# Performance work log

Measured on AMD Instinct MI355X. Metric: run time of the kernel, lower is better.

Reference implementation:

```python
import jax, jax.numpy as jnp
import numpy as np

# MLABlock dims (from __init__ defaults / chosen init_kwargs)
B, S, D = 2, 2048, 2048
H = 16
NOPE, ROPE, VD = 128, 64, 128
KVR = 512
NE, TOPK = 12, 4
EI, SEI = 1024, 2048
THETA = 10000.0
MSCALE = 1.0
EPS = 1e-6


def setup_inputs() -> dict:
    key = jax.random.key(0)
    ks = jax.random.split(key, 14)
    w = lambda k, shp: jax.random.normal(k, shp, jnp.float32) * 0.02
    return {
        "x": jax.random.normal(ks[0], (B, S, D), jnp.float32),
        "start_pos": 0,
        "norm_w": jnp.ones((D,), jnp.float32),
        "wq": w(ks[1], (H * (NOPE + ROPE), D)),
        "wkv_a": w(ks[2], (KVR + ROPE, D)),
        "kv_norm_w": jnp.ones((KVR,), jnp.float32),
        "wkv_b": w(ks[3], (H * (NOPE + VD), KVR)),
        "wo": w(ks[4], (D, H * VD)),
        "gate_w": w(ks[5], (NE, D)),
        "gate_bias": w(ks[6], (NE,)),
        "w1": w(ks[7], (NE, EI, D)),
        "w2": w(ks[8], (NE, D, EI)),
        "w3": w(ks[9], (NE, EI, D)),
        "sw1": w(ks[10], (SEI, D)),
        "sw2": w(ks[11], (D, SEI)),
        "sw3": w(ks[12], (SEI, D)),
    }


def _rms(v, w):
    return v * jax.lax.rsqrt(jnp.mean(v * v, -1, keepdims=True) + EPS) * w


def reference(x, start_pos, norm_w, wq, wkv_a, kv_norm_w, wkv_b, wo,
              gate_w, gate_bias, w1, w2, w3, sw1, sw2, sw3):
    b, s, d = x.shape
    # ---- MLA attention sub-layer ----
    h = _rms(x, norm_w)
    q = (h @ wq.T).reshape(b, s, H, NOPE + ROPE)
    q_nope, q_pe = q[..., :NOPE], q[..., NOPE:]
    kv = h @ wkv_a.T                      # [b,s,KVR+ROPE]
    kv_lat, k_pe = kv[..., :KVR], kv[..., KVR:]
    # rotary embedding (interleaved pairs), positions start_pos..start_pos+s
    pos = jnp.arange(s, dtype=jnp.float32) + start_pos
    inv = 1.0 / (THETA ** (jnp.arange(0, ROPE, 2, dtype=jnp.float32) / ROPE))
    ang = pos[:, None] * inv              # [s, ROPE/2]
    cos = jnp.cos(ang)[None, :, None, :]
    sin = jnp.sin(ang)[None, :, None, :]
    def rot(t):                           # t: [b,s,h,ROPE]
        t1, t2 = t[..., 0::2], t[..., 1::2]
        return jnp.stack([t1 * cos - t2 * sin, t1 * sin + t2 * cos], -1).reshape(t.shape)
    q_pe = rot(q_pe)
    k_pe = rot(k_pe[:, :, None, :])       # [b,s,1,ROPE] shared across heads
    kv_lat = _rms(kv_lat, kv_norm_w)
    kvb = (kv_lat @ wkv_b.T).reshape(b, s, H, NOPE + VD)
    k_nope, v = kvb[..., :NOPE], kvb[..., NOPE:]
    k = jnp.concatenate([k_nope, jnp.broadcast_to(k_pe, (b, s, H, ROPE))], -1)
    qf = jnp.concatenate([q_nope, q_pe], -1)
    scale = MSCALE * (NOPE + ROPE) ** -0.5
    mask = jnp.triu(jnp.full((s, s), -1e9, x.dtype), 1)  # causal
    scores = jnp.einsum('bqhd,bkhd->bhqk', qf, k) * scale + mask
    attn = jax.nn.softmax(scores, -1)
    o = jnp.einsum('bhqk,bkhd->bqhd', attn, v).reshape(b, s, H * VD) @ wo.T
    first = o + x
    # ---- MoE sub-layer (shared self.norm reused) ----
    h2 = _rms(first, norm_w)
    g_scores = jax.nn.sigmoid(h2 @ gate_w.T)             # [b,s,NE]
    _, idx = jax.lax.top_k(g_scores + gate_bias, TOPK)   # adaptive-bias selection
    gw = jnp.take_along_axis(g_scores, idx, -1)          # weights from raw scores
    gw = gw / jnp.sum(gw, -1, keepdims=True)
    out = (jax.nn.silu(h2 @ sw1.T) * (h2 @ sw3.T)) @ sw2.T  # shared expert
    for e in range(NE):                                  # fixed small expert set
        we = jnp.sum(jnp.where(idx == e, gw, 0.0), -1)   # [b,s]
        ye = (jax.nn.silu(h2 @ w1[e].T) * (h2 @ w3[e].T)) @ w2[e].T
        out = out + we[..., None] * ye
    return out + first
```

## Files before the change

### kernel.cpp

```cpp
#include <hip/hip_runtime.h>
#include <cstdint>
#include <cstddef>
#include <cmath>

#define DI __device__ __forceinline__
typedef float f32x4 __attribute__((ext_vector_type(4)));
typedef __bf16 bf16x8 __attribute__((ext_vector_type(8)));
typedef unsigned short u16;
typedef unsigned int u32;

static constexpr int TKN = 4096, SEQ = 2048, DIM = 2048, NH = 16;

DI u16 f2bf(float f) {
  union { float f; u32 u; } v; v.f = f;
  u32 r = v.u + 0x7fffu + ((v.u >> 16) & 1u);
  return (u16)(r >> 16);
}
DI float bf2f(u16 h) {
  union { u32 u; float f; } v; v.u = ((u32)h) << 16;
  return v.f;
}
DI f32x4 mfma16(bf16x8 a, bf16x8 b, f32x4 c) {
  return __builtin_amdgcn_mfma_f32_16x16x32_bf16(a, b, c, 0, 0, 0);
}
DI void gld16(const u16* g, u16* l) {
  __builtin_amdgcn_global_load_lds((const __attribute__((address_space(1))) u32*)g,
                                   (__attribute__((address_space(3))) u32*)l, 16, 0, 0);
}

enum { EF_F32 = 0, EF_BF16 = 1, EF_RES = 2, EF_KV = 3, EF_SILU = 4, EF_ATOM = 5, EF_QROPE = 6 };
enum { AM_DIR = 0, AM_LIST = 1, AM_OFF = 2 };

template<int EPI, int AMODE, int NSEG>
__global__ __launch_bounds__(256)
void gemm_f(const u16* __restrict__ A, const u16* __restrict__ B, void* __restrict__ C,
            int M, int N, int K, size_t apl, size_t bpl,
            const int* __restrict__ list, const int* __restrict__ basep,
            const int* __restrict__ counts,
            const void* __restrict__ aux, const float* __restrict__ gws,
            u16* __restrict__ kd0, u16* __restrict__ kd1, u16* __restrict__ vT,
            const float* __restrict__ cosT)
{
  constexpr int BM = 128, BK = 64;
  __shared__ __align__(16) u16 As[BM * BK];
  __shared__ __align__(16) u16 Bs[BM * BK];
  int rowbase = 0;
  if (AMODE != AM_DIR) {
    int z = blockIdx.z;
    M = counts[z];
    rowbase = basep[z];
    B += (size_t)z * (size_t)N * K;
  }
  int m0 = blockIdx.x * BM, n0 = blockIdx.y * BM;
  if (m0 >= M) return;
  int tid = threadIdx.x, lane = tid & 63, wid = tid >> 6;
  int wm = (wid >> 1) * 64, wn = (wid & 1) * 64;
  int lr = lane & 15, lk = (lane >> 4) * 8;

  const u16* asrc[4];
  const u16* bsrc[4];
  int l8 = lane >> 3, c8 = ((lane & 7) ^ l8) * 8;
  #pragma unroll
  for (int i = 0; i < 4; i++) {
    int chunk = wid * 4 + i;
    int ra = m0 + chunk * 8 + l8;
    size_t rowidx;
    if (AMODE == AM_LIST)      rowidx = (size_t)list[rowbase + (ra < M ? ra : 0)];
    else if (AMODE == AM_OFF)  rowidx = (size_t)(rowbase + (ra < M ? ra : 0));
    else                       rowidx = (size_t)ra;
    asrc[i] = A + rowidx * (size_t)K + c8;
    int rb = n0 + chunk * 8 + l8;
    if (rb >= N) rb = N - 1;
    bsrc[i] = B + (size_t)rb * K + c8;
  }

  f32x4 acc[4][4] = {};
  int sw = lr & 7;
  #pragma unroll 1
  for (int s = 0; s < NSEG; s++) {
    int sa = (s == 4) ? 2 : (s & 1);
    int sb = (s == 5) ? 2 : ((s >> 1) & 1);
    size_t ao = (size_t)sa * apl, bo = (size_t)sb * bpl;
    for (int kt = 0; kt < K; kt += BK) {
      #pragma unroll
      for (int i = 0; i < 4; i++) {
        gld16(asrc[i] + ao + kt, &As[(wid * 4 + i) * 512]);
        gld16(bsrc[i] + bo + kt, &Bs[(wid * 4 + i) * 512]);
      }
      __syncthreads();
      #pragma unroll
      for (int ko = 0; ko < BK; ko += 32) {
        bf16x8 af[4], bv[4];
        int sl = ((((ko + lk) >> 3) ^ sw) << 3);
        #pragma unroll
        for (int i = 0; i < 4; i++)
          af[i] = *(const bf16x8*)(&As[(wm + i * 16 + lr) * 64 + sl]);
        #pragma unroll
        for (int j = 0; j < 4; j++)
          bv[j] = *(const bf16x8*)(&Bs[(wn + j * 16 + lr) * 64 + sl]);
        #pragma unroll
        for (int i = 0; i < 4; i++)
          #pragma unroll
          for (int j = 0; j < 4; j++)
            acc[i][j] = mfma16(af[i], bv[j], acc[i][j]);
      }
      __syncthreads();
    }
  }

  int og = (lane >> 4) * 4;
  #pragma unroll
  for (int i = 0; i < 4; i++)
    #pragma unroll
    for (int p = 0; p < 4; p++) {
      int r = m0 + wm + i * 16 + og + p;
      if (EPI != EF_QROPE && EPI != EF_KV) { if (r >= M) continue; }
      size_t outr = (AMODE == AM_DIR) ? (size_t)r : (size_t)(rowbase + r);
      #pragma unroll
      for (int j = 0; j < 4; j++) {
        int c = n0 + wn + j * 16 + lr;
        float v = acc[i][j][p];
        if (EPI == EF_F32) {
          if (c < N) ((float*)C)[outr * N + c] = v;
        } else if (EPI == EF_BF16) {
          ((u16*)C)[outr * N + c] = f2bf(v);
        } else if (EPI == EF_RES) {
          ((float*)C)[outr * N + c] = v + ((const float*)aux)[outr * N + c];
        } else if (EPI == EF_SILU) {
          float t = bf2f(((const u16*)aux)[outr * N + c]);
          float sg = t / (1.f + __expf(-t));
          ((u16*)C)[outr * N + c] = f2bf(sg * v);
        } else if (EPI == EF_ATOM) {
          int tok = list[outr];
          float w = gws[outr];
          atomicAdd((float*)C + (size_t)tok * N + c, w * v);
        } else if (EPI == EF_QROPE) {
          int wi = c % 192;
          float vo = v;
          if (wi >= 128) {
            float part = __shfl_xor(v, 1);
            int jj = (wi - 128) >> 1;
            int srow = r & (SEQ - 1);
            float cs = cosT[srow * 32 + jj];
            float sn = ((const float*)aux)[srow * 32 + jj];
            vo = (c & 1) ? (part * sn + v * cs) : (v * cs - part * sn);
          }
          u16 b0 = f2bf(vo);
          u16 b1 = f2bf(vo - bf2f(b0));
          kd0[outr * (size_t)N + c] = b0;
          kd1[outr * (size_t)N + c] = b1;
        } else if (EPI == EF_KV) {
          int hd = c >> 8, cc = c & 255;
          u16 b0 = f2bf(v);
          float r1 = v - bf2f(b0);
          u16 b1 = f2bf(r1);
          if (cc < 128) {
            size_t base = ((size_t)r * NH + hd) * 128 + cc;
            kd0[base] = b0; kd1[base] = b1;
          } else {
            u16 b2 = f2bf(r1 - bf2f(b1));
            int bb = r >> 11, ss = r & (SEQ - 1);
            constexpr size_t VPL = (size_t)32 * 128 * 2048;
            size_t vb = ((size_t)((bb * 16 + hd) * 128 + (cc - 128))) * 2048 + ss;
            vT[vb] = b0; vT[VPL + vb] = b1; vT[2 * VPL + vb] = b2;
          }
        }
      }
    }
}

__global__ __launch_bounds__(256)
void attn3(const u16* __restrict__ q0p, const u16* __restrict__ q1p,
           const u16* __restrict__ k0p, const u16* __restrict__ k1p,
           const u16* __restrict__ kp0, const u16* __restrict__ kp1,
           const u16* __restrict__ vT, u16* __restrict__ o0, float scale)
{
  constexpr int KLD = 200, VLD = 40, PLD = 36;
  constexpr size_t VPL = (size_t)32 * 128 * 2048;
  constexpr size_t OPL = (size_t)TKN * DIM;
  __shared__ __align__(16) u16 Ks[2][32 * KLD];
  __shared__ __align__(16) u16 Vt[3][128 * VLD];
  __shared__ __align__(16) float Ps[4][16 * PLD];

  int bh = blockIdx.y;
  int b = bh >> 4, h = bh & 15;
  int tid = threadIdx.x, lane = tid & 63, wid = tid >> 6;
  int lr = lane & 15, lg = lane >> 4, lk = lg * 8;
  size_t tbase = (size_t)b * SEQ;
  const u16* vbase = vT + (size_t)bh * 128 * 2048;

  for (int half = 0; half < 2; half++) {
    int qt = half ? (31 - (int)blockIdx.x) : (int)blockIdx.x;
    int q0r = qt * 64;
    bf16x8 qf[2][6];
    {
      size_t qoff = (tbase + q0r + wid * 16 + lr) * (size_t)3072 + h * 192;
      #pragma unroll
      for (int kc = 0; kc < 6; kc++) {
        qf[0][kc] = *(const bf16x8*)(q0p + qoff + kc * 32 + lk);
        qf[1][kc] = *(const bf16x8*)(q1p + qoff + kc * 32 + lk);
      }
    }
    f32x4 oacc[8] = {};
    float mrow[4], lrow[4];
    #pragma unroll
    for (int p = 0; p < 4; p++) { mrow[p] = -1e30f; lrow[p] = 0.f; }

    int nkt = 2 * qt + 2;
    for (int kt = 0; kt < nkt; kt++) {
      __syncthreads();
      int kr0 = kt * 32;
      #pragma unroll
      for (int p = 0; p < 2; p++) {
        const u16* knp = p ? k1p : k0p;
        const u16* kpp = p ? kp1 : kp0;
        #pragma unroll
        for (int i = 0; i < 2; i++) {
          int vv = tid + i * 256, r = vv >> 4, cc8 = (vv & 15) * 8;
          int4 d = *(const int4*)(knp + ((tbase + kr0 + r) * (size_t)NH + h) * 128 + cc8);
          *(int4*)(&Ks[p][r * KLD + cc8]) = d;
        }
        {
          int r = tid >> 3, cc8 = (tid & 7) * 8;
          int4 d = *(const int4*)(kpp + (tbase + kr0 + r) * (size_t)64 + cc8);
          *(int4*)(&Ks[p][r * KLD + 128 + cc8]) = d;
        }
      }
      #pragma unroll
      for (int p = 0; p < 3; p++) {
        #pragma unroll
        for (int i = 0; i < 2; i++) {
          int vv = tid + i * 256, d = vv >> 2, cc8 = (vv & 3) * 8;
          int4 dd = *(const int4*)(vbase + p * VPL + (size_t)d * 2048 + kr0 + cc8);
          *(int4*)(&Vt[p][d * VLD + cc8]) = dd;
        }
      }
      __syncthreads();

      f32x4 sacc[2] = {};
      #pragma unroll
      for (int j = 0; j < 2; j++)
        #pragma unroll
        for (int kc = 0; kc < 6; kc++) {
          bf16x8 kf0 = *(const bf16x8*)(&Ks[0][(j * 16 + lr) * KLD + kc * 32 + lk]);
          bf16x8 kf1 = *(const bf16x8*)(&Ks[1][(j * 16 + lr) * KLD + kc * 32 + lk]);
          f32x4 t = sacc[j];
          t = mfma16(qf[0][kc], kf0, t);
          t = mfma16(qf[1][kc], kf0, t);
          t = mfma16(qf[0][kc], kf1, t);
          sacc[j] = t;
        }

      bool tail = (kt >= 2 * qt);
      float fsc[4];
      #pragma unroll
      for (int p = 0; p < 4; p++) {
        float s0 = sacc[0][p] * scale, s1 = sacc[1][p] * scale;
        if (tail) {
          int qrow = q0r + wid * 16 + lg * 4 + p;
          if (kr0 + lr > qrow) s0 = -1e30f;
          if (kr0 + 16 + lr > qrow) s1 = -1e30f;
        }
        float mx = fmaxf(s0, s1);
        #pragma unroll
        for (int off = 1; off < 16; off <<= 1) mx = fmaxf(mx, __shfl_xor(mx, off));
        float mnew = fmaxf(mrow[p], mx);
        fsc[p] = __expf(mrow[p] - mnew);
        float e0 = __expf(s0 - mnew), e1 = __expf(s1 - mnew);
        float ssum = e0 + e1;
        #pragma unroll
        for (int off = 1; off < 16; off <<= 1) ssum += __shfl_xor(ssum, off);
        lrow[p] = lrow[p] * fsc[p] + ssum;
        mrow[p] = mnew;
        Ps[wid][(lg * 4 + p) * PLD + lr] = e0;
        Ps[wid][(lg * 4 + p) * PLD + 16 + lr] = e1;
      }
      #pragma unroll
      for (int jf = 0; jf < 8; jf++) {
        f32x4 t = oacc[jf];
        t[0] *= fsc[0]; t[1] *= fsc[1]; t[2] *= fsc[2]; t[3] *= fsc[3];
        oacc[jf] = t;
      }

      f32x4 pva = *(const f32x4*)(&Ps[wid][lr * PLD + lk]);
      f32x4 pvb = *(const f32x4*)(&Ps[wid][lr * PLD + lk + 4]);
      union { u16 us[8]; bf16x8 v; } pa0u, pa1u;
      #pragma unroll
      for (int e = 0; e < 4; e++) {
        float va = pva[e];
        u16 b0 = f2bf(va); pa0u.us[e] = b0; pa1u.us[e] = f2bf(va - bf2f(b0));
        float vb = pvb[e];
        u16 c0 = f2bf(vb); pa0u.us[4 + e] = c0; pa1u.us[4 + e] = f2bf(vb - bf2f(c0));
      }

      #pragma unroll
      for (int jf = 0; jf < 8; jf++) {
        bf16x8 vf0 = *(const bf16x8*)(&Vt[0][(jf * 16 + lr) * VLD + lk]);
        bf16x8 vf1 = *(const bf16x8*)(&Vt[1][(jf * 16 + lr) * VLD + lk]);
        bf16x8 vf2 = *(const bf16x8*)(&Vt[2][(jf * 16 + lr) * VLD + lk]);
        f32x4 t = oacc[jf];
        t = mfma16(pa0u.v, vf0, t);
        t = mfma16(pa1u.v, vf0, t);
        t = mfma16(pa0u.v, vf1, t);
        t = mfma16(pa1u.v, vf1, t);
        t = mfma16(pa0u.v, vf2, t);
        oacc[jf] = t;
      }
    }

    #pragma unroll
    for (int p = 0; p < 4; p++) {
      float inv = 1.f / lrow[p];
      int qrow = q0r + wid * 16 + lg * 4 + p;
      size_t base = (tbase + qrow) * (size_t)DIM + h * 128;
      #pragma unroll
      for (int jf = 0; jf < 8; jf++) {
        float val = oacc[jf][p] * inv;
        u16 b0 = f2bf(val);
        float r1 = val - bf2f(b0);
        u16 b1 = f2bf(r1);
        u16 b2 = f2bf(r1 - bf2f(b1));
        size_t idx = base + jf * 16 + lr;
        o0[idx] = b0; o0[OPL + idx] = b1; o0[2 * OPL + idx] = b2;
      }
    }
  }
}

__global__ __launch_bounds__(256)
void rmsnorm3(const float* __restrict__ x, const float* __restrict__ w, u16* __restrict__ out)
{
  __shared__ float sred[4];
  constexpr size_t PL = (size_t)TKN * DIM;
  int t = blockIdx.x, tid = threadIdx.x;
  const float* xp = x + (size_t)t * DIM;
  float vals[8], ss = 0.f;
  #pragma unroll
  for (int i = 0; i < 8; i++) { float v = xp[tid + i * 256]; vals[i] = v; ss += v * v; }
  #pragma unroll
  for (int off = 32; off > 0; off >>= 1) ss += __shfl_xor(ss, off);
  if ((tid & 63) == 0) sred[tid >> 6] = ss;
  __syncthreads();
  ss = sred[0] + sred[1] + sred[2] + sred[3];
  float rstd = 1.f / sqrtf(ss / (float)DIM + 1e-6f);
  #pragma unroll
  for (int i = 0; i < 8; i++) {
    int d = tid + i * 256;
    float v = vals[i] * rstd * w[d];
    u16 b0 = f2bf(v);
    float r1 = v - bf2f(b0);
    u16 b1 = f2bf(r1);
    u16 b2 = f2bf(r1 - bf2f(b1));
    size_t o = (size_t)t * DIM + d;
    out[o] = b0; out[PL + o] = b1; out[2 * PL + o] = b2;
  }
}

__global__ __launch_bounds__(256)
void rmsnorm1(const float* __restrict__ x, const float* __restrict__ w, u16* __restrict__ out)
{
  __shared__ float sred[4];
  int t = blockIdx.x, tid = threadIdx.x;
  const float* xp = x + (size_t)t * DIM;
  float vals[8], ss = 0.f;
  #pragma unroll
  for (int i = 0; i < 8; i++) { float v = xp[tid + i * 256]; vals[i] = v; ss += v * v; }
  #pragma unroll
  for (int off = 32; off > 0; off >>= 1) ss += __shfl_xor(ss, off);
  if ((tid & 63) == 0) sred[tid >> 6] = ss;
  __syncthreads();
  ss = sred[0] + sred[1] + sred[2] + sred[3];
  float rstd = 1.f / sqrtf(ss / (float)DIM + 1e-6f);
  #pragma unroll
  for (int i = 0; i < 8; i++) {
    int d = tid + i * 256;
    out[(size_t)t * DIM + d] = f2bf(vals[i] * rstd * w[d]);
  }
}

__global__ __launch_bounds__(256)
void split3(const float* __restrict__ src, u16* __restrict__ dst, size_t n, size_t pl)
{
  size_t i0 = ((size_t)blockIdx.x * 256 + threadIdx.x) * 4;
  size_t stride = (size_t)gridDim.x * 1024;
  for (size_t i = i0; i < n; i += stride) {
    float4 d = *(const float4*)(src + i);
    ushort4 b0, b1, b2; float r;
    b0.x = f2bf(d.x); r = d.x - bf2f(b0.x); b1.x = f2bf(r); b2.x = f2bf(r - bf2f(b1.x));
    b0.y = f2bf(d.y); r = d.y - bf2f(b0.y); b1.y = f2bf(r); b2.y = f2bf(r - bf2f(b1.y));
    b0.z = f2bf(d.z); r = d.z - bf2f(b0.z); b1.z = f2bf(r); b2.z = f2bf(r - bf2f(b1.z));
    b0.w = f2bf(d.w); r = d.w - bf2f(b0.w); b1.w = f2bf(r); b2.w = f2bf(r - bf2f(b1.w));
    *(ushort4*)(dst + i) = b0;
    *(ushort4*)(dst + pl + i) = b1;
    *(ushort4*)(dst + 2 * pl + i) = b2;
  }
}

__global__ __launch_bounds__(256)
void cvt1(const float* __restrict__ src, u16* __restrict__ dst, size_t n)
{
  size_t i0 = ((size_t)blockIdx.x * 256 + threadIdx.x) * 4;
  size_t stride = (size_t)gridDim.x * 1024;
  for (size_t i = i0; i < n; i += stride) {
    float4 d = *(const float4*)(src + i);
    ushort4 b;
    b.x = f2bf(d.x); b.y = f2bf(d.y); b.z = f2bf(d.z); b.w = f2bf(d.w);
    *(ushort4*)(dst + i) = b;
  }
}

__global__ __launch_bounds__(256)
void kv_split(const float* __restrict__ kvraw, const float* __restrict__ kvw,
              u16* __restrict__ c0, u16* __restrict__ kp0, u16* __restrict__ kp1,
              const float* __restrict__ cosT, const float* __restrict__ sinT)
{
  __shared__ float sred[4];
  constexpr size_t CPL = (size_t)TKN * 512;
  int t = blockIdx.x, tid = threadIdx.x;
  const float* xp = kvraw + (size_t)t * 576;
  float v0 = xp[tid], v1 = xp[tid + 256];
  float ss = v0 * v0 + v1 * v1;
  #pragma unroll
  for (int off = 32; off > 0; off >>= 1) ss += __shfl_xor(ss, off);
  if ((tid & 63) == 0) sred[tid >> 6] = ss;
  __syncthreads();
  ss = sred[0] + sred[1] + sred[2] + sred[3];
  float rstd = 1.f / sqrtf(ss / 512.f + 1e-6f);
  #pragma unroll
  for (int half = 0; half < 2; half++) {
    float v = (half ? v1 : v0) * rstd * kvw[tid + half * 256];
    u16 b0 = f2bf(v);
    float r1 = v - bf2f(b0);
    u16 b1 = f2bf(r1);
    u16 b2 = f2bf(r1 - bf2f(b1));
    size_t o = (size_t)t * 512 + tid + half * 256;
    c0[o] = b0; c0[CPL + o] = b1; c0[2 * CPL + o] = b2;
  }
  if (tid < 32) {
    int srow = t & (SEQ - 1);
    float a = xp[512 + tid * 2], bb = xp[512 + tid * 2 + 1];
    float cs = cosT[srow * 32 + tid], sn = sinT[srow * 32 + tid];
    float ra = a * cs - bb * sn, rb = a * sn + bb * cs;
    u16 a0 = f2bf(ra), a1 = f2bf(ra - bf2f(a0));
    u16 c0b = f2bf(rb), c1 = f2bf(rb - bf2f(c0b));
    kp0[(size_t)t * 64 + tid * 2] = a0;     kp1[(size_t)t * 64 + tid * 2] = a1;
    kp0[(size_t)t * 64 + tid * 2 + 1] = c0b; kp1[(size_t)t * 64 + tid * 2 + 1] = c1;
  }
}

__global__ __launch_bounds__(256)
void rope_table(float* __restrict__ cosT, float* __restrict__ sinT, const int* __restrict__ sp)
{
  int i = blockIdx.x * 256 + threadIdx.x;
  if (i >= SEQ * 32) return;
  int j = i & 31, srow = i >> 5;
  float pos = (float)(srow + sp[0]);
  float inv = powf(10000.f, -(float)(2 * j) / 64.f);
  cosT[i] = cosf(pos * inv);
  sinT[i] = sinf(pos * inv);
}

__global__ __launch_bounds__(256)
void gate_topk(const float* __restrict__ first, const float* __restrict__ nw,
               const float* __restrict__ gwm, const float* __restrict__ gbias,
               int* __restrict__ idx, float* __restrict__ gw4, int* __restrict__ counts)
{
  __shared__ float sred[4];
  __shared__ float sacc[12][4];
  int t = blockIdx.x, tid = threadIdx.x;
  const float* xp = first + (size_t)t * DIM;
  float vals[8], ss = 0.f;
  #pragma unroll
  for (int i = 0; i < 8; i++) { float v = xp[tid + i * 256]; vals[i] = v; ss += v * v; }
  #pragma unroll
  for (int off = 32; off > 0; off >>= 1) ss += __shfl_xor(ss, off);
  if ((tid & 63) == 0) sred[tid >> 6] = ss;
  __syncthreads();
  ss = sred[0] + sred[1] + sred[2] + sred[3];
  float rstd = 1.f / sqrtf(ss / (float)DIM + 1e-6f);
  float acc[12];
  #pragma unroll
  for (int e = 0; e < 12; e++) acc[e] = 0.f;
  #pragma unroll
  for (int i = 0; i < 8; i++) {
    int d = tid + i * 256;
    float v = vals[i] * rstd * nw[d];
    #pragma unroll
    for (int e = 0; e < 12; e++) acc[e] += v * gwm[e * DIM + d];
  }
  #pragma unroll
  for (int e = 0; e < 12; e++) {
    float a = acc[e];
    #pragma unroll
    for (int off = 32; off > 0; off >>= 1) a += __shfl_xor(a, off);
    if ((tid & 63) == 0) sacc[e][tid >> 6] = a;
  }
  __syncthreads();
  if (tid == 0) {
    float g[12], sc[12];
    #pragma unroll
    for (int e = 0; e < 12; e++) {
      float s = sacc[e][0] + sacc[e][1] + sacc[e][2] + sacc[e][3];
      g[e] = 1.f / (1.f + __expf(-s));
      sc[e] = g[e] + gbias[e];
    }
    bool taken[12] = {};
    int sel[4];
    float wsum = 0.f;
    #pragma unroll
    for (int s4 = 0; s4 < 4; s4++) {
      float best = -1e38f; int bi = 0;
      for (int e = 0; e < 12; e++)
        if (!taken[e] && sc[e] > best) { best = sc[e]; bi = e; }
      taken[bi] = true; sel[s4] = bi; wsum += g[bi];
    }
    #pragma unroll
    for (int s4 = 0; s4 < 4; s4++) {
      idx[t * 4 + s4] = sel[s4];
      gw4[t * 4 + s4] = g[sel[s4]] / wsum;
      atomicAdd(&counts[sel[s4]], 1);
    }
  }
}

__global__ void prefix12(const int* __restrict__ counts, int* __restrict__ basep,
                         int* __restrict__ cursor)
{
  if (threadIdx.x == 0) {
    int run = 0;
    for (int e = 0; e < 12; e++) { basep[e] = run; run += counts[e]; cursor[e] = 0; }
  }
}

__global__ __launch_bounds__(256)
void fill_lists(const int* __restrict__ idx, const int* __restrict__ basep,
                int* __restrict__ cursor, int* __restrict__ list,
                const float* __restrict__ gw4, float* __restrict__ gws)
{
  int t = blockIdx.x * 256 + threadIdx.x;
  if (t >= TKN) return;
  #pragma unroll
  for (int s = 0; s < 4; s++) {
    int e = idx[t * 4 + s];
    int pos = atomicAdd(&cursor[e], 1);
    list[basep[e] + pos] = t;
    gws[basep[e] + pos] = gw4[t * 4 + s];
  }
}

__global__ __launch_bounds__(256)
void final_add(float* __restrict__ out, const float* __restrict__ first)
{
  size_t i0 = ((size_t)blockIdx.x * 256 + threadIdx.x) * 4;
  size_t stride = (size_t)gridDim.x * 1024;
  size_t n = (size_t)TKN * DIM;
  for (size_t i = i0; i < n; i += stride) {
    float4 a = *(const float4*)(out + i);
    float4 b = *(const float4*)(first + i);
    a.x += b.x; a.y += b.y; a.z += b.z; a.w += b.w;
    *(float4*)(out + i) = a;
  }
}

extern "C" void kernel_launch(void* const* d_in, const int* in_sizes, int n_in,
                              void* d_out, int out_size, void* d_ws, size_t ws_size,
                              hipStream_t stream)
{
  (void)in_sizes; (void)n_in; (void)out_size; (void)ws_size;
  const float* x      = (const float*)d_in[0];
  const int*   sp     = (const int*)d_in[1];
  const float* norm_w = (const float*)d_in[2];
  const float* wq     = (const float*)d_in[3];
  const float* wkv_a  = (const float*)d_in[4];
  const float* kvnw   = (const float*)d_in[5];
  const float* wkv_b  = (const float*)d_in[6];
  const float* wo     = (const float*)d_in[7];
  const float* gatew  = (const float*)d_in[8];
  const float* gateb  = (const float*)d_in[9];
  const float* w1     = (const float*)d_in[10];
  const float* w2     = (const float*)d_in[11];
  const float* w3     = (const float*)d_in[12];
  const float* sw1    = (const float*)d_in[13];
  const float* sw2    = (const float*)d_in[14];
  const float* sw3    = (const float*)d_in[15];
  float* out = (float*)d_out;
  char* ws = (char*)d_ws;

  const size_t D0 = 0, D1 = 50331648ull, D2 = 100663296ull, D3 = 150994944ull;
  const size_t SM = 188743680ull;
  u16* hpl   = (u16*)(ws + D0);
  u16* cpl   = (u16*)(ws + D0);
  u16* wkvbp = (u16*)(ws + D0 + 12582912ull);
  u16* opl   = (u16*)(ws + D0);
  u16* t1b   = (u16*)(ws + D0);
  u16* asb   = (u16*)(ws + D0 + 16777216ull);
  u16* aeb   = (u16*)(ws + D0);
  u16* qpl   = (u16*)(ws + D1);
  u16* wexp  = (u16*)(ws + D1);
  u16* swp   = (u16*)(ws + D1 + 25165824ull);
  u16* vtp   = (u16*)(ws + D2);
  float* firstb = (float*)(ws + D2);
  u16* h2b   = (u16*)(ws + D2 + 33554432ull);
  u16* wqp   = (u16*)(ws + D3);
  u16* wkvap = (u16*)(ws + D3);
  float* kvr = (float*)(ws + D3 + 7077888ull);
  u16* kpl0  = (u16*)(ws + D3);
  u16* kpl1  = kpl0 + 8388608ull;
  u16* kpe0  = (u16*)(ws + D3 + 33554432ull);
  u16* kpe1  = kpe0 + 262144ull;
  u16* wop   = (u16*)(ws + D3);
  u16* y1eb  = (u16*)(ws + D3);
  float* cosT = (float*)(ws + SM);
  float* sinT = (float*)(ws + SM + 262144ull);
  int*   idxb = (int*)(ws + SM + 524288ull);
  float* gw4b = (float*)(ws + SM + 589824ull);
  int*   listb= (int*)(ws + SM + 655360ull);
  float* gwsb = (float*)(ws + SM + 720896ull);
  int*   cntb = (int*)(ws + SM + 786432ull);
  int*   curb = (int*)(ws + SM + 786688ull);
  int*   baseb= (int*)(ws + SM + 786944ull);

  const size_t PL_TD = (size_t)TKN * DIM;

  hipMemsetAsync(cntb, 0, 256, stream);
  rope_table<<<dim3(256), 256, 0, stream>>>(cosT, sinT, sp);
  rmsnorm3<<<dim3(TKN), 256, 0, stream>>>(x, norm_w, hpl);

  split3<<<dim3(1024), 256, 0, stream>>>(wq, wqp, (size_t)3072 * 2048, 6291456ull);
  gemm_f<EF_QROPE, AM_DIR, 3><<<dim3(32, 24), 256, 0, stream>>>(
      hpl, wqp, nullptr, TKN, 3072, 2048, PL_TD, 6291456ull,
      nullptr, nullptr, nullptr, sinT, nullptr, qpl, qpl + 12582912ull, nullptr, cosT);

  split3<<<dim3(512), 256, 0, stream>>>(wkv_a, wkvap, (size_t)576 * 2048, 1179648ull);
  gemm_f<EF_F32, AM_DIR, 6><<<dim3(32, 5), 256, 0, stream>>>(
      hpl, wkvap, kvr, TKN, 576, 2048, PL_TD, 1179648ull,
      nullptr, nullptr, nullptr, nullptr, nullptr, nullptr, nullptr, nullptr, nullptr);

  kv_split<<<dim3(TKN), 256, 0, stream>>>(kvr, kvnw, cpl, kpe0, kpe1, cosT, sinT);

  split3<<<dim3(1024), 256, 0, stream>>>(wkv_b, wkvbp, (size_t)4096 * 512, 2097152ull);
  gemm_f<EF_KV, AM_DIR, 6><<<dim3(32, 32), 256, 0, stream>>>(
      cpl, wkvbp, nullptr, TKN, 4096, 512, 2097152ull, 2097152ull,
      nullptr, nullptr, nullptr, nullptr, nullptr, kpl0, kpl1, vtp, nullptr);

  attn3<<<dim3(16, 32), 256, 0, stream>>>(qpl, qpl + 12582912ull, kpl0, kpl1,
      kpe0, kpe1, vtp, opl, 1.f / sqrtf(192.f));

  split3<<<dim3(1024), 256, 0, stream>>>(wo, wop, (size_t)2048 * 2048, 4194304ull);
  gemm_f<EF_RES, AM_DIR, 6><<<dim3(32, 16), 256, 0, stream>>>(
      opl, wop, firstb, TKN, 2048, 2048, PL_TD, 4194304ull,
      nullptr, nullptr, nullptr, x, nullptr, nullptr, nullptr, nullptr, nullptr);

  rmsnorm1<<<dim3(TKN), 256, 0, stream>>>(firstb, norm_w, h2b);
  gate_topk<<<dim3(TKN), 256, 0, stream>>>(firstb, norm_w, gatew, gateb, idxb, gw4b, cntb);
  prefix12<<<dim3(1), 64, 0, stream>>>(cntb, baseb, curb);
  fill_lists<<<dim3(16), 256, 0, stream>>>(idxb, baseb, curb, listb, gw4b, gwsb);

  cvt1<<<dim3(1024), 256, 0, stream>>>(sw1, swp, (size_t)2048 * 2048);
  cvt1<<<dim3(1024), 256, 0, stream>>>(sw3, swp + 4194304ull, (size_t)2048 * 2048);
  cvt1<<<dim3(1024), 256, 0, stream>>>(sw2, swp + 8388608ull, (size_t)2048 * 2048);
  gemm_f<EF_BF16, AM_DIR, 1><<<dim3(32, 16), 256, 0, stream>>>(
      h2b, swp, t1b, TKN, 2048, 2048, 0, 0,
      nullptr, nullptr, nullptr, nullptr, nullptr, nullptr, nullptr, nullptr, nullptr);
  gemm_f<EF_SILU, AM_DIR, 1><<<dim3(32, 16), 256, 0, stream>>>(
      h2b, swp + 4194304ull, asb, TKN, 2048, 2048, 0, 0,
      nullptr, nullptr, nullptr, t1b, nullptr, nullptr, nullptr, nullptr, nullptr);
  gemm_f<EF_F32, AM_DIR, 1><<<dim3(32, 16), 256, 0, stream>>>(
      asb, swp + 8388608ull, out, TKN, 2048, 2048, 0, 0,
      nullptr, nullptr, nullptr, nullptr, nullptr, nullptr, nullptr, nullptr, nullptr);

  for (int g = 0; g < 2; g++) {
    cvt1<<<dim3(2048), 256, 0, stream>>>(w1 + (size_t)g * 6 * 1024 * 2048, wexp,
                                         (size_t)6 * 1024 * 2048);
    gemm_f<EF_BF16, AM_LIST, 1><<<dim3(32, 8, 6), 256, 0, stream>>>(
        h2b, wexp, y1eb, 0, 1024, 2048, 0, 0,
        listb, baseb + g * 6, cntb + g * 6, nullptr, nullptr, nullptr, nullptr, nullptr, nullptr);
    cvt1<<<dim3(2048), 256, 0, stream>>>(w3 + (size_t)g * 6 * 1024 * 2048, wexp,
                                         (size_t)6 * 1024 * 2048);
    gemm_f<EF_SILU, AM_LIST, 1><<<dim3(32, 8, 6), 256, 0, stream>>>(
        h2b, wexp, aeb, 0, 1024, 2048, 0, 0,
        listb, baseb + g * 6, cntb + g * 6, y1eb, nullptr, nullptr, nullptr, nullptr, nullptr);
    cvt1<<<dim3(2048), 256, 0, stream>>>(w2 + (size_t)g * 6 * 2048 * 1024, wexp,
                                         (size_t)6 * 2048 * 1024);
    gemm_f<EF_ATOM, AM_OFF, 1><<<dim3(32, 16, 6), 256, 0, stream>>>(
        aeb, wexp, out, 0, 2048, 1024, 0, 0,
        listb, baseb + g * 6, cntb + g * 6, nullptr, gwsb, nullptr, nullptr, nullptr, nullptr);
  }

  final_add<<<dim3(2048), 256, 0, stream>>>(out, firstb);
}
```

Before: 2.432 ms.

## Enlarge attention query tiles and fuse MoE rmsnorm and residual add

The attention kernel now runs 512 threads per block with 128-row query tiles, so each staged K/V tile is shared by eight waves instead of four, and the grid shrinks to 8x32. The separate rmsnorm1 kernel is removed because gate_topk now writes the bf16 normalized activations as well. The final_add kernel is removed by having the shared-expert down-projection use the residual epilogue with firstb. The larger attention blocks cut grid size and may lower occupancy or worsen load balance.

```diff
diff --git a/kernel.cpp b/kernel.cpp
--- a/kernel.cpp
+++ b/kernel.cpp
@@ -169,7 +169,7 @@
     }
 }
 
-__global__ __launch_bounds__(256)
+__global__ __launch_bounds__(512)
 void attn3(const u16* __restrict__ q0p, const u16* __restrict__ q1p,
            const u16* __restrict__ k0p, const u16* __restrict__ k1p,
            const u16* __restrict__ kp0, const u16* __restrict__ kp1,
@@ -180,7 +180,7 @@
   constexpr size_t OPL = (size_t)TKN * DIM;
   __shared__ __align__(16) u16 Ks[2][32 * KLD];
   __shared__ __align__(16) u16 Vt[3][128 * VLD];
-  __shared__ __align__(16) float Ps[4][16 * PLD];
+  __shared__ __align__(16) float Ps[8][16 * PLD];
 
   int bh = blockIdx.y;
   int b = bh >> 4, h = bh & 15;
@@ -190,8 +190,8 @@
   const u16* vbase = vT + (size_t)bh * 128 * 2048;
 
   for (int half = 0; half < 2; half++) {
-    int qt = half ? (31 - (int)blockIdx.x) : (int)blockIdx.x;
-    int q0r = qt * 64;
+    int qt = half ? (15 - (int)blockIdx.x) : (int)blockIdx.x;
+    int q0r = qt * 128;
     bf16x8 qf[2][6];
     {
       size_t qoff = (tbase + q0r + wid * 16 + lr) * (size_t)3072 + h * 192;
@@ -206,34 +206,29 @@
     #pragma unroll
     for (int p = 0; p < 4; p++) { mrow[p] = -1e30f; lrow[p] = 0.f; }
 
-    int nkt = 2 * qt + 2;
+    int nkt = 4 * qt + 4;
     for (int kt = 0; kt < nkt; kt++) {
       __syncthreads();
       int kr0 = kt * 32;
       #pragma unroll
-      for (int p = 0; p < 2; p++) {
-        const u16* knp = p ? k1p : k0p;
-        const u16* kpp = p ? kp1 : kp0;
-        #pragma unroll
-        for (int i = 0; i < 2; i++) {
-          int vv = tid + i * 256, r = vv >> 4, cc8 = (vv & 15) * 8;
-          int4 d = *(const int4*)(knp + ((tbase + kr0 + r) * (size_t)NH + h) * 128 + cc8);
-          *(int4*)(&Ks[p][r * KLD + cc8]) = d;
-        }
-        {
-          int r = tid >> 3, cc8 = (tid & 7) * 8;
-          int4 d = *(const int4*)(kpp + (tbase + kr0 + r) * (size_t)64 + cc8);
-          *(int4*)(&Ks[p][r * KLD + 128 + cc8]) = d;
-        }
+      for (int i = 0; i < 2; i++) {
+        const u16* knp = i ? k1p : k0p;
+        int r = tid >> 4, cc8 = (tid & 15) * 8;
+        int4 d = *(const int4*)(knp + ((tbase + kr0 + r) * (size_t)NH + h) * 128 + cc8);
+        *(int4*)(&Ks[i][r * KLD + cc8]) = d;
+      }
+      {
+        const u16* kpp = (tid & 256) ? kp1 : kp0;
+        int pp = (tid >> 8) & 1;
+        int r = (tid >> 3) & 31, cc8 = (tid & 7) * 8;
+        int4 d = *(const int4*)(kpp + (tbase + kr0 + r) * (size_t)64 + cc8);
+        *(int4*)(&Ks[pp][r * KLD + 128 + cc8]) = d;
       }
       #pragma unroll
       for (int p = 0; p < 3; p++) {
-        #pragma unroll
-        for (int i = 0; i < 2; i++) {
-          int vv = tid + i * 256, d = vv >> 2, cc8 = (vv & 3) * 8;
-          int4 dd = *(const int4*)(vbase + p * VPL + (size_t)d * 2048 + kr0 + cc8);
-          *(int4*)(&Vt[p][d * VLD + cc8]) = dd;
-        }
+        int d = tid >> 2, cc8 = (tid & 3) * 8;
+        int4 dd = *(const int4*)(vbase + p * VPL + (size_t)d * 2048 + kr0 + cc8);
+        *(int4*)(&Vt[p][d * VLD + cc8]) = dd;
       }
       __syncthreads();
 
@@ -251,7 +246,7 @@
           sacc[j] = t;
         }
 
-      bool tail = (kt >= 2 * qt);
+      bool tail = (kt >= 4 * qt);
       float fsc[4];
       #pragma unroll
       for (int p = 0; p < 4; p++) {
@@ -357,28 +352,6 @@
 }
 
 __global__ __launch_bounds__(256)
-void rmsnorm1(const float* __restrict__ x, const float* __restrict__ w, u16* __restrict__ out)
-{
-  __shared__ float sred[4];
-  int t = blockIdx.x, tid = threadIdx.x;
-  const float* xp = x + (size_t)t * DIM;
-  float vals[8], ss = 0.f;
-  #pragma unroll
-  for (int i = 0; i < 8; i++) { float v = xp[tid + i * 256]; vals[i] = v; ss += v * v; }
-  #pragma unroll
-  for (int off = 32; off > 0; off >>= 1) ss += __shfl_xor(ss, off);
-  if ((tid & 63) == 0) sred[tid >> 6] = ss;
-  __syncthreads();
-  ss = sred[0] + sred[1] + sred[2] + sred[3];
-  float rstd = 1.f / sqrtf(ss / (float)DIM + 1e-6f);
-  #pragma unroll
-  for (int i = 0; i < 8; i++) {
-    int d = tid + i * 256;
-    out[(size_t)t * DIM + d] = f2bf(vals[i] * rstd * w[d]);
-  }
-}
-
-__global__ __launch_bounds__(256)
 void split3(const float* __restrict__ src, u16* __restrict__ dst, size_t n, size_t pl)
 {
   size_t i0 = ((size_t)blockIdx.x * 256 + threadIdx.x) * 4;
@@ -463,7 +436,8 @@
 __global__ __launch_bounds__(256)
 void gate_topk(const float* __restrict__ first, const float* __restrict__ nw,
                const float* __restrict__ gwm, const float* __restrict__ gbias,
-               int* __restrict__ idx, float* __restrict__ gw4, int* __restrict__ counts)
+               int* __restrict__ idx, float* __restrict__ gw4, int* __restrict__ counts,
+               u16* __restrict__ h2out)
 {
   __shared__ float sred[4];
   __shared__ float sacc[12][4];
@@ -485,6 +459,7 @@
   for (int i = 0; i < 8; i++) {
     int d = tid + i * 256;
     float v = vals[i] * rstd * nw[d];
+    h2out[(size_t)t * DIM + d] = f2bf(v);
     #pragma unroll
     for (int e = 0; e < 12; e++) acc[e] += v * gwm[e * DIM + d];
   }
@@ -545,20 +520,6 @@
     int pos = atomicAdd(&cursor[e], 1);
     list[basep[e] + pos] = t;
     gws[basep[e] + pos] = gw4[t * 4 + s];
-  }
-}
-
-__global__ __launch_bounds__(256)
-void final_add(float* __restrict__ out, const float* __restrict__ first)
-{
-  size_t i0 = ((size_t)blockIdx.x * 256 + threadIdx.x) * 4;
-  size_t stride = (size_t)gridDim.x * 1024;
-  size_t n = (size_t)TKN * DIM;
-  for (size_t i = i0; i < n; i += stride) {
-    float4 a = *(const float4*)(out + i);
-    float4 b = *(const float4*)(first + i);
-    a.x += b.x; a.y += b.y; a.z += b.z; a.w += b.w;
-    *(float4*)(out + i) = a;
   }
 }
 
@@ -643,7 +604,7 @@
       cpl, wkvbp, nullptr, TKN, 4096, 512, 2097152ull, 2097152ull,
       nullptr, nullptr, nullptr, nullptr, nullptr, kpl0, kpl1, vtp, nullptr);
 
-  attn3<<<dim3(16, 32), 256, 0, stream>>>(qpl, qpl + 12582912ull, kpl0, kpl1,
+  attn3<<<dim3(8, 32), 512, 0, stream>>>(qpl, qpl + 12582912ull, kpl0, kpl1,
       kpe0, kpe1, vtp, opl, 1.f / sqrtf(192.f));
 
   split3<<<dim3(1024), 256, 0, stream>>>(wo, wop, (size_t)2048 * 2048, 4194304ull);
@@ -651,8 +612,7 @@
       opl, wop, firstb, TKN, 2048, 2048, PL_TD, 4194304ull,
       nullptr, nullptr, nullptr, x, nullptr, nullptr, nullptr, nullptr, nullptr);
 
-  rmsnorm1<<<dim3(TKN), 256, 0, stream>>>(firstb, norm_w, h2b);
-  gate_topk<<<dim3(TKN), 256, 0, stream>>>(firstb, norm_w, gatew, gateb, idxb, gw4b, cntb);
+  gate_topk<<<dim3(TKN), 256, 0, stream>>>(firstb, norm_w, gatew, gateb, idxb, gw4b, cntb, h2b);
   prefix12<<<dim3(1), 64, 0, stream>>>(cntb, baseb, curb);
   fill_lists<<<dim3(16), 256, 0, stream>>>(idxb, baseb, curb, listb, gw4b, gwsb);
 
@@ -665,9 +625,9 @@
   gemm_f<EF_SILU, AM_DIR, 1><<<dim3(32, 16), 256, 0, stream>>>(
       h2b, swp + 4194304ull, asb, TKN, 2048, 2048, 0, 0,
       nullptr, nullptr, nullptr, t1b, nullptr, nullptr, nullptr, nullptr, nullptr);
-  gemm_f<EF_F32, AM_DIR, 1><<<dim3(32, 16), 256, 0, stream>>>(
+  gemm_f<EF_RES, AM_DIR, 1><<<dim3(32, 16), 256, 0, stream>>>(
       asb, swp + 8388608ull, out, TKN, 2048, 2048, 0, 0,
-      nullptr, nullptr, nullptr, nullptr, nullptr, nullptr, nullptr, nullptr, nullptr);
+      nullptr, nullptr, nullptr, firstb, nullptr, nullptr, nullptr, nullptr, nullptr);
 
   for (int g = 0; g < 2; g++) {
     cvt1<<<dim3(2048), 256, 0, stream>>>(w1 + (size_t)g * 6 * 1024 * 2048, wexp,
@@ -686,6 +646,4 @@
         aeb, wexp, out, 0, 2048, 1024, 0, 0,
         listb, baseb + g * 6, cntb + g * 6, nullptr, gwsb, nullptr, nullptr, nullptr, nullptr);
   }
-
-  final_add<<<dim3(2048), 256, 0, stream>>>(out, firstb);
-}
+}
```

After: 2.441 ms. Within noise of the previous version (+0.4%).

## Fuse RMSNorm into gate, residual into shared GEMM, add lazy softmax rescale

Applied to the files above, without the earlier changes.

The separate rmsnorm1 kernel is folded into gate_topk, which now also writes the bf16 normalized activations. The final_add pass is dropped by switching the shared-expert down-projection epilogue to add the residual directly. In attention, the online softmax skips rescaling the accumulator when the running max has grown by no more than a threshold, and the MFMA loops are wrapped in s_setprio. Together these remove two full-tensor memory passes and some per-tile exp/multiply work. The cost is a wave-wide vote and a divergent branch in the attention loop.

```diff
diff --git a/kernel.cpp b/kernel.cpp
--- a/kernel.cpp
+++ b/kernel.cpp
@@ -238,6 +238,7 @@
       __syncthreads();
 
       f32x4 sacc[2] = {};
+      __builtin_amdgcn_s_setprio(1);
       #pragma unroll
       for (int j = 0; j < 2; j++)
         #pragma unroll
@@ -250,9 +251,11 @@
           t = mfma16(qf[0][kc], kf1, t);
           sacc[j] = t;
         }
+      __builtin_amdgcn_s_setprio(0);
 
       bool tail = (kt >= 2 * qt);
-      float fsc[4];
+      float sv0[4], sv1[4], mxv[4];
+      float need = 0.f;
       #pragma unroll
       for (int p = 0; p < 4; p++) {
         float s0 = sacc[0][p] * scale, s1 = sacc[1][p] * scale;
@@ -264,22 +267,42 @@
         float mx = fmaxf(s0, s1);
         #pragma unroll
         for (int off = 1; off < 16; off <<= 1) mx = fmaxf(mx, __shfl_xor(mx, off));
-        float mnew = fmaxf(mrow[p], mx);
-        fsc[p] = __expf(mrow[p] - mnew);
-        float e0 = __expf(s0 - mnew), e1 = __expf(s1 - mnew);
-        float ssum = e0 + e1;
-        #pragma unroll
-        for (int off = 1; off < 16; off <<= 1) ssum += __shfl_xor(ssum, off);
-        lrow[p] = lrow[p] * fsc[p] + ssum;
-        mrow[p] = mnew;
-        Ps[wid][(lg * 4 + p) * PLD + lr] = e0;
-        Ps[wid][(lg * 4 + p) * PLD + 16 + lr] = e1;
-      }
-      #pragma unroll
-      for (int jf = 0; jf < 8; jf++) {
-        f32x4 t = oacc[jf];
-        t[0] *= fsc[0]; t[1] *= fsc[1]; t[2] *= fsc[2]; t[3] *= fsc[3];
-        oacc[jf] = t;
+        sv0[p] = s0; sv1[p] = s1; mxv[p] = mx;
+        need = fmaxf(need, mx - mrow[p]);
+      }
+      bool stable = __all(need <= 8.f);
+      if (stable) {
+        #pragma unroll
+        for (int p = 0; p < 4; p++) {
+          float e0 = __expf(sv0[p] - mrow[p]), e1 = __expf(sv1[p] - mrow[p]);
+          float ssum = e0 + e1;
+          #pragma unroll
+          for (int off = 1; off < 16; off <<= 1) ssum += __shfl_xor(ssum, off);
+          lrow[p] += ssum;
+          Ps[wid][(lg * 4 + p) * PLD + lr] = e0;
+          Ps[wid][(lg * 4 + p) * PLD + 16 + lr] = e1;
+        }
+      } else {
+        float fsc[4];
+        #pragma unroll
+        for (int p = 0; p < 4; p++) {
+          float mnew = fmaxf(mrow[p], mxv[p]);
+          fsc[p] = __expf(mrow[p] - mnew);
+          float e0 = __expf(sv0[p] - mnew), e1 = __expf(sv1[p] - mnew);
+          float ssum = e0 + e1;
+          #pragma unroll
+          for (int off = 1; off < 16; off <<= 1) ssum += __shfl_xor(ssum, off);
+          lrow[p] = lrow[p] * fsc[p] + ssum;
+          mrow[p] = mnew;
+          Ps[wid][(lg * 4 + p) * PLD + lr] = e0;
+          Ps[wid][(lg * 4 + p) * PLD + 16 + lr] = e1;
+        }
+        #pragma unroll
+        for (int jf = 0; jf < 8; jf++) {
+          f32x4 t = oacc[jf];
+          t[0] *= fsc[0]; t[1] *= fsc[1]; t[2] *= fsc[2]; t[3] *= fsc[3];
+          oacc[jf] = t;
+        }
       }
 
       f32x4 pva = *(const f32x4*)(&Ps[wid][lr * PLD + lk]);
@@ -293,6 +316,7 @@
         u16 c0 = f2bf(vb); pa0u.us[4 + e] = c0; pa1u.us[4 + e] = f2bf(vb - bf2f(c0));
       }
 
+      __builtin_amdgcn_s_setprio(1);
       #pragma unroll
       for (int jf = 0; jf < 8; jf++) {
         bf16x8 vf0 = *(const bf16x8*)(&Vt[0][(jf * 16 + lr) * VLD + lk]);
@@ -306,6 +330,7 @@
         t = mfma16(pa0u.v, vf2, t);
         oacc[jf] = t;
       }
+      __builtin_amdgcn_s_setprio(0);
     }
 
     #pragma unroll
@@ -353,28 +378,6 @@
     u16 b2 = f2bf(r1 - bf2f(b1));
     size_t o = (size_t)t * DIM + d;
     out[o] = b0; out[PL + o] = b1; out[2 * PL + o] = b2;
-  }
-}
-
-__global__ __launch_bounds__(256)
-void rmsnorm1(const float* __restrict__ x, const float* __restrict__ w, u16* __restrict__ out)
-{
-  __shared__ float sred[4];
-  int t = blockIdx.x, tid = threadIdx.x;
-  const float* xp = x + (size_t)t * DIM;
-  float vals[8], ss = 0.f;
-  #pragma unroll
-  for (int i = 0; i < 8; i++) { float v = xp[tid + i * 256]; vals[i] = v; ss += v * v; }
-  #pragma unroll
-  for (int off = 32; off > 0; off >>= 1) ss += __shfl_xor(ss, off);
-  if ((tid & 63) == 0) sred[tid >> 6] = ss;
-  __syncthreads();
-  ss = sred[0] + sred[1] + sred[2] + sred[3];
-  float rstd = 1.f / sqrtf(ss / (float)DIM + 1e-6f);
-  #pragma unroll
-  for (int i = 0; i < 8; i++) {
-    int d = tid + i * 256;
-    out[(size_t)t * DIM + d] = f2bf(vals[i] * rstd * w[d]);
   }
 }
 
@@ -463,7 +466,8 @@
 __global__ __launch_bounds__(256)
 void gate_topk(const float* __restrict__ first, const float* __restrict__ nw,
                const float* __restrict__ gwm, const float* __restrict__ gbias,
-               int* __restrict__ idx, float* __restrict__ gw4, int* __restrict__ counts)
+               int* __restrict__ idx, float* __restrict__ gw4, int* __restrict__ counts,
+               u16* __restrict__ h2out)
 {
   __shared__ float sred[4];
   __shared__ float sacc[12][4];
@@ -485,6 +489,7 @@
   for (int i = 0; i < 8; i++) {
     int d = tid + i * 256;
     float v = vals[i] * rstd * nw[d];
+    h2out[(size_t)t * DIM + d] = f2bf(v);
     #pragma unroll
     for (int e = 0; e < 12; e++) acc[e] += v * gwm[e * DIM + d];
   }
@@ -545,20 +550,6 @@
     int pos = atomicAdd(&cursor[e], 1);
     list[basep[e] + pos] = t;
     gws[basep[e] + pos] = gw4[t * 4 + s];
-  }
-}
-
-__global__ __launch_bounds__(256)
-void final_add(float* __restrict__ out, const float* __restrict__ first)
-{
-  size_t i0 = ((size_t)blockIdx.x * 256 + threadIdx.x) * 4;
-  size_t stride = (size_t)gridDim.x * 1024;
-  size_t n = (size_t)TKN * DIM;
-  for (size_t i = i0; i < n; i += stride) {
-    float4 a = *(const float4*)(out + i);
-    float4 b = *(const float4*)(first + i);
-    a.x += b.x; a.y += b.y; a.z += b.z; a.w += b.w;
-    *(float4*)(out + i) = a;
   }
 }
 
@@ -651,8 +642,7 @@
       opl, wop, firstb, TKN, 2048, 2048, PL_TD, 4194304ull,
       nullptr, nullptr, nullptr, x, nullptr, nullptr, nullptr, nullptr, nullptr);
 
-  rmsnorm1<<<dim3(TKN), 256, 0, stream>>>(firstb, norm_w, h2b);
-  gate_topk<<<dim3(TKN), 256, 0, stream>>>(firstb, norm_w, gatew, gateb, idxb, gw4b, cntb);
+  gate_topk<<<dim3(TKN), 256, 0, stream>>>(firstb, norm_w, gatew, gateb, idxb, gw4b, cntb, h2b);
   prefix12<<<dim3(1), 64, 0, stream>>>(cntb, baseb, curb);
   fill_lists<<<dim3(16), 256, 0, stream>>>(idxb, baseb, curb, listb, gw4b, gwsb);
 
@@ -665,9 +655,9 @@
   gemm_f<EF_SILU, AM_DIR, 1><<<dim3(32, 16), 256, 0, stream>>>(
       h2b, swp + 4194304ull, asb, TKN, 2048, 2048, 0, 0,
       nullptr, nullptr, nullptr, t1b, nullptr, nullptr, nullptr, nullptr, nullptr);
-  gemm_f<EF_F32, AM_DIR, 1><<<dim3(32, 16), 256, 0, stream>>>(
+  gemm_f<EF_RES, AM_DIR, 1><<<dim3(32, 16), 256, 0, stream>>>(
       asb, swp + 8388608ull, out, TKN, 2048, 2048, 0, 0,
-      nullptr, nullptr, nullptr, nullptr, nullptr, nullptr, nullptr, nullptr, nullptr);
+      nullptr, nullptr, nullptr, firstb, nullptr, nullptr, nullptr, nullptr, nullptr);
 
   for (int g = 0; g < 2; g++) {
     cvt1<<<dim3(2048), 256, 0, stream>>>(w1 + (size_t)g * 6 * 1024 * 2048, wexp,
@@ -686,6 +676,4 @@
         aeb, wexp, out, 0, 2048, 1024, 0, 0,
         listb, baseb + g * 6, cntb + g * 6, nullptr, gwsb, nullptr, nullptr, nullptr, nullptr);
   }
-
-  final_add<<<dim3(2048), 256, 0, stream>>>(out, firstb);
-}
+}
```

Measured after the change: 2.513 ms. 3.3% more time.
